# Optimization experiments

Measured on AMD Instinct MI355X. Metric: run time of the kernel, lower is better.

Reference implementation:

```python
import jax, jax.numpy as jnp
import numpy as np

B, W_DIM, CIN, COUT, K, H = 16, 512, 512, 512, 3, 64
PAD = (K - 1) // 2          # conv padding, also filtered_lrelu padding
GAIN = float(np.sqrt(2.0))  # lrelu gain (not torgb)
SLOPE = 0.2                 # lrelu slope (not torgb)
CLAMP = 256.0               # conv_clamp
AFFINE_WG = float(1.0 / np.sqrt(W_DIM))  # FullyConnectedLayer weight_gain


def setup_inputs() -> dict:
    key = jax.random.key(0)
    k0, k1, k2, k3 = jax.random.split(key, 4)
    return {
        "x": jax.random.normal(k0, (B, CIN, H, H), jnp.float32),
        "w": jax.random.normal(k1, (B, W_DIM), jnp.float32),
        "affine_weight": jax.random.normal(k2, (CIN, W_DIM), jnp.float32),
        "affine_bias": jnp.ones((CIN,), jnp.float32),       # bias_init=1
        "conv_weight": jax.random.normal(k3, (COUT, CIN, K, K), jnp.float32),
        "bias": jnp.zeros((COUT,), jnp.float32),
        "magnitude_ema": jnp.ones((), jnp.float32),
    }


def reference(x, w, affine_weight, affine_bias, conv_weight, bias, magnitude_ema):
    input_gain = jax.lax.rsqrt(magnitude_ema)
    # --- affine (FullyConnectedLayer, linear act, lr_mult=1) ---
    s = w @ (affine_weight * AFFINE_WG).T + affine_bias          # [B, CIN]
    # --- modulated_conv2d with demodulation (is_torgb=False) ---
    wk = conv_weight * jax.lax.rsqrt(
        jnp.mean(jnp.square(conv_weight), axis=(1, 2, 3), keepdims=True))
    s = s * jax.lax.rsqrt(jnp.mean(jnp.square(s)))
    wb = wk[None] * s[:, None, :, None, None]                    # [B,COUT,CIN,K,K]
    dcoefs = jax.lax.rsqrt(jnp.sum(jnp.square(wb), axis=(2, 3, 4)) + 1e-8)  # [B,COUT]
    wb = wb * dcoefs[:, :, None, None, None] * input_gain
    # grouped conv: groups = batch, one weight set per sample
    xg = x.reshape(1, B * CIN, H, H)
    wg = wb.reshape(B * COUT, CIN, K, K)
    y = jax.lax.conv_general_dilated(
        xg, wg, window_strides=(1, 1), padding=[(PAD, PAD), (PAD, PAD)],
        dimension_numbers=("NCHW", "OIHW", "NCHW"), feature_group_count=B)
    y = y.reshape(B, COUT, H, H)
    # --- filtered_lrelu: up=down=1, fu=fd=None (identity FIR) ---
    # => bias add, zero-pad by `padding`, lrelu * gain, clamp
    y = y + bias[:, None, None]
    y = jnp.pad(y, ((0, 0), (0, 0), (PAD, PAD), (PAD, PAD)))
    y = jnp.where(y >= 0, y, y * SLOPE) * GAIN
    y = jnp.clip(y, -CLAMP, CLAMP)                               # [B,COUT,66,66]
    return y
```

## Files before the change

### kernel.cpp

```cpp
#include <hip/hip_runtime.h>

#define B_     16
#define WDIM   512
#define CIN_   512
#define COUT_  512
#define HH     64
#define KC     32
#define NCHUNK (CIN_/KC)
#define AFFINE_WG 0.044194173824159216f
#define GAIN_  1.4142135623730951f
#define CLAMP_ 256.0f

#define WBYTES 36864
#define XBYTES 42240
#define BUFBYTES (WBYTES + XBYTES)

typedef __attribute__((ext_vector_type(4))) float f32x4;
typedef __attribute__((ext_vector_type(8))) short bf16x8;
typedef __attribute__((ext_vector_type(8))) unsigned short u16x8;

__device__ __forceinline__ unsigned short f2bf(float f) {
    union { float f; unsigned u; } un; un.f = f;
    unsigned u = un.u;
    u += 0x7FFFu + ((u >> 16) & 1u);
    return (unsigned short)(u >> 16);
}

__device__ __forceinline__ void gl_lds16(const void* g, void* l) {
    __builtin_amdgcn_global_load_lds(
        reinterpret_cast<const __attribute__((address_space(1))) unsigned int*>(
            reinterpret_cast<uintptr_t>(g)),
        reinterpret_cast<__attribute__((address_space(3))) unsigned int*>(
            reinterpret_cast<uintptr_t>(l)),
        16, 0, 0);
}


__global__ void k_affine(const float* __restrict__ w, const float* __restrict__ aw,
                         const float* __restrict__ ab, float* __restrict__ s,
                         float* __restrict__ part) {
    const int tid = threadIdx.x;
    const int b = blockIdx.x >> 1;
    const int c = ((blockIdx.x & 1) << 8) + tid;
    const f32x4* wr = (const f32x4*)(w + (size_t)b * WDIM);
    const f32x4* ar = (const f32x4*)(aw + (size_t)c * WDIM);
    float acc = 0.f;
    #pragma unroll 4
    for (int k = 0; k < WDIM / 4; ++k) {
        f32x4 a = ar[k], bb = wr[k];
        acc += a[0]*bb[0] + a[1]*bb[1] + a[2]*bb[2] + a[3]*bb[3];
    }
    float sv = acc * AFFINE_WG + ab[c];
    s[b * CIN_ + c] = sv;
    __shared__ float red[256];
    red[tid] = sv * sv;
    __syncthreads();
    for (int off = 128; off > 0; off >>= 1) {
        if (tid < off) red[tid] += red[tid + off];
        __syncthreads();
    }
    if (tid == 0) part[blockIdx.x] = red[0];
}

__global__ void k_wnorm(const float* __restrict__ cw, float* __restrict__ alpha,
                        float* __restrict__ Q) {
    const int o = blockIdx.x;
    const int tid = threadIdx.x;
    __shared__ float qsh[512];
    __shared__ float red[256];
    __shared__ float a_sh;
    float tot = 0.f;
    #pragma unroll
    for (int half = 0; half < 2; ++half) {
        const int c = tid + half * 256;
        const float* p = cw + ((size_t)o * 512 + c) * 9;
        float qs = 0.f;
        #pragma unroll
        for (int t = 0; t < 9; ++t) { float v = p[t]; qs += v * v; }
        qsh[c] = qs; tot += qs;
    }
    red[tid] = tot; __syncthreads();
    for (int off = 128; off > 0; off >>= 1) {
        if (tid < off) red[tid] += red[tid + off];
        __syncthreads();
    }
    if (tid == 0) { a_sh = rsqrtf(red[0] * (1.0f / 4608.0f)); alpha[o] = a_sh; }
    __syncthreads();
    const float a2 = a_sh * a_sh;
    Q[(size_t)o * 512 + tid]       = a2 * qsh[tid];
    Q[(size_t)o * 512 + tid + 256] = a2 * qsh[tid + 256];
}

__global__ void k_g(const float* __restrict__ s, const float* __restrict__ part,
                    const float* __restrict__ Q, const float* __restrict__ alpha,
                    const float* __restrict__ ema, float* __restrict__ g) {
    const int tid = threadIdx.x;
    const int b = blockIdx.x >> 1;
    const int o = ((blockIdx.x & 1) << 8) + tid;
    __shared__ float rs2_sh;
    if (tid == 0) {
        float t = 0.f;
        #pragma unroll
        for (int i = 0; i < 32; ++i) t += part[i];
        rs2_sh = 8192.0f / t;
    }
    __syncthreads();
    const f32x4* sh = (const f32x4*)(s + (size_t)b * CIN_);
    const f32x4* qq = (const f32x4*)(Q + (size_t)o * CIN_);
    float d = 0.f;
    #pragma unroll 4
    for (int k = 0; k < CIN_ / 4; ++k) {
        f32x4 a = sh[k], q4 = qq[k];
        d += a[0]*a[0]*q4[0] + a[1]*a[1]*q4[1] + a[2]*a[2]*q4[2] + a[3]*a[3]*q4[3];
    }
    const float ig = rsqrtf(ema[0]);
    g[b * COUT_ + o] = alpha[o] * rsqrtf(d * rs2_sh + 1e-8f) * ig;
}

__global__ void k_wprep2(const float* __restrict__ cw, unsigned short* __restrict__ wb) {
    const int S = blockIdx.x * 256 + threadIdx.x;
    const int p    = S / 2304;
    const int srem = S - p * 2304;
    const int a    = srem * 16;
    const int tap  = a >> 12;
    const int o    = (a >> 6) & 63;
    const int c0   = ((a & 63) ^ ((o & 6) << 3)) >> 1;
    const int ot = p >> 4, cc = p & 15;
    const int og = ot * 64 + o;
    const int cg = cc * 32 + c0;
    const float* src = cw + ((size_t)og * 512 + cg) * 9 + tap;
    u16x8 v;
    #pragma unroll
    for (int j = 0; j < 8; ++j) v[j] = f2bf(src[j * 9]);
    *(u16x8*)(wb + (size_t)S * 8) = v;
}

__global__ void k_xprep(const float* __restrict__ x, const float* __restrict__ s,
                        const float* __restrict__ part, unsigned short* __restrict__ xbf) {
    __shared__ float rs_sh;
    if (threadIdx.x == 0) {
        float t = 0.f;
        #pragma unroll
        for (int i = 0; i < 32; ++i) t += part[i];
        rs_sh = rsqrtf(t * (1.0f / 8192.0f));
    }
    __syncthreads();
    const float rs = rs_sh;
    const int slot = blockIdx.x * 256 + threadIdx.x;
    const int pair = slot >> 14;
    const int rem  = slot & 16383;
    const int row  = rem >> 8;
    const int ro16 = rem & 255;
    const int full = ro16 * 16 + 64;
    const int col  = full >> 6;
    const int c0   = ((full & 63) ^ ((col & 6) << 3)) >> 1;
    const int b    = pair >> 4, cc = pair & 15;
    const int cbase = cc * 32 + c0;
    const float* src = x + (((size_t)(b * CIN_ + cbase)) * HH + row) * HH + (col - 1);
    const float* sp  = s + b * CIN_ + cbase;
    u16x8 v;
    #pragma unroll
    for (int j = 0; j < 8; ++j)
        v[j] = f2bf(src[(size_t)j * 4096] * (sp[j] * rs));
    *(u16x8*)(xbf + (size_t)slot * 8) = v;
}

__global__ void k_border2(float* __restrict__ out) {
    const int f = blockIdx.x * 256 + threadIdx.x;
    const int bo = f / 132;
    const int r = f - bo * 132;
    const int row = (r >= 66) ? 65 : 0;
    const int col = (r >= 66) ? (r - 66) : r;
    out[(size_t)bo * 4356 + row * 66 + col] = 0.f;
}

__global__ __launch_bounds__(512, 2) void k_conv3(
    const unsigned short* __restrict__ xbf, const unsigned short* __restrict__ wb,
    const float* __restrict__ g, const float* __restrict__ bias,
    float* __restrict__ out) {
    __shared__ char lds[2 * BUFBYTES];

    const int tid  = threadIdx.x;
    const int lane = tid & 63;
    const int wv   = tid >> 6;
    const int l15  = lane & 15;
    const int hi   = lane >> 4;
    const int b  = blockIdx.z;
    const int ot = blockIdx.y;
    const int rt = blockIdx.x;
    const int h0 = rt * 8;

    const f32x4 zero4 = {0.f, 0.f, 0.f, 0.f};
    f32x4 acc[4][4];
    #pragma unroll
    for (int i = 0; i < 4; ++i)
        #pragma unroll
        for (int j = 0; j < 4; ++j) acc[i][j] = zero4;

    {
        unsigned int* x0 = (unsigned int*)(lds + WBYTES);
        unsigned int* x1 = (unsigned int*)(lds + BUFBYTES + WBYTES);
        for (int i = tid; i < XBYTES / 4; i += 512) { x0[i] = 0u; x1[i] = 0u; }
    }
    __syncthreads();

    const char* wsrc0 = (const char*)wb + (size_t)ot * 16 * WBYTES;
    const char* xsrc0 = (const char*)xbf + (size_t)b * 16 * 262144;

    auto STAGE = [&](int cc, char* base) {
        if (tid < 256) {
            const char* wsrc = wsrc0 + (size_t)cc * WBYTES;
            #pragma unroll
            for (int r = 0; r < 9; ++r)
                gl_lds16(wsrc + r * 4096 + tid * 16, base + r * 4096 + tid * 16);
        } else {
            const int t2 = tid - 256;
            const char* xsrc = xsrc0 + (size_t)cc * 262144;
            char* xb = base + WBYTES;
            #pragma unroll
            for (int r = 0; r < 10; ++r) {
                const int h_in = h0 - 1 + r;
                if ((unsigned)h_in < 64u)
                    gl_lds16(xsrc + (size_t)h_in * 4096 + t2 * 16,
                             xb + r * 4224 + 64 + t2 * 16);
            }
        }
    };

    STAGE(0, lds);
    __syncthreads();
    int cur = 0;

    for (int cc = 0; cc < NCHUNK; ++cc) {
        char* cbase = lds + cur * BUFBYTES;
        if (cc + 1 < NCHUNK) STAGE(cc + 1, lds + (cur ^ 1) * BUFBYTES);

        const char* Wl = cbase;
        const char* Xl = cbase + WBYTES;
        #pragma unroll
        for (int tap = 0; tap < 9; ++tap) {
            const int ti = tap / 3, tj = tap - ti * 3;
            bf16x8 af[4];
            #pragma unroll
            for (int mi = 0; mi < 4; ++mi) {
                const int o = mi * 16 + l15;
                int byte = (tap << 12) + (o << 6) + (hi << 4);
                byte ^= ((o & 6) << 3);
                af[mi] = *(const bf16x8*)(Wl + byte);
            }
            bf16x8 bg[4];
            const int row = wv + ti;
            #pragma unroll
            for (int ni = 0; ni < 4; ++ni) {
                const int col = ni * 16 + l15 + tj;
                int byte = (((row * 66 + col) << 5) + (hi << 3)) << 1;
                byte ^= ((col & 6) << 3);
                bg[ni] = *(const bf16x8*)(Xl + byte);
            }
            #pragma unroll
            for (int mi = 0; mi < 4; ++mi)
                #pragma unroll
                for (int ni = 0; ni < 4; ++ni)
                    acc[mi][ni] = __builtin_amdgcn_mfma_f32_16x16x32_bf16(
                        af[mi], bg[ni], acc[mi][ni], 0, 0, 0);
        }
        __syncthreads();
        cur ^= 1;
    }

    {
        const int obase = ot * 64;
        const int orow = h0 + wv + 1;
        #pragma unroll
        for (int mi = 0; mi < 4; ++mi) {
            #pragma unroll
            for (int r = 0; r < 4; ++r) {
                const int o = obase + mi * 16 + hi * 4 + r;
                const float gg = g[b * COUT_ + o];
                const float bb = bias[o];
                float* op = out + ((size_t)(b * COUT_ + o) * 66 + orow) * 66;
                #pragma unroll
                for (int ni = 0; ni < 4; ++ni) {
                    float v = acc[mi][ni][r] * gg + bb;
                    v = (v >= 0.f ? v : v * 0.2f) * GAIN_;
                    v = fminf(fmaxf(v, -CLAMP_), CLAMP_);
                    op[ni * 16 + l15 + 1] = v;
                }
                if (l15 == 0)  op[0]  = 0.f;
                if (l15 == 15) op[65] = 0.f;
            }
        }
    }
}

extern "C" void kernel_launch(void* const* d_in, const int* in_sizes, int n_in,
                              void* d_out, int out_size, void* d_ws, size_t ws_size,
                              hipStream_t stream) {
    const float* x    = (const float*)d_in[0];
    const float* w    = (const float*)d_in[1];
    const float* aw   = (const float*)d_in[2];
    const float* ab   = (const float*)d_in[3];
    const float* cw   = (const float*)d_in[4];
    const float* bias = (const float*)d_in[5];
    const float* ema  = (const float*)d_in[6];
    float* out = (float*)d_out;

    float* wsf   = (float*)d_ws;
    float* s     = wsf;
    float* part  = wsf + 8192;
    float* alpha = wsf + 16512;
    float* Q     = wsf + 17024;
    float* g     = wsf + 279168;
    unsigned short* wb  = (unsigned short*)((char*)d_ws + 1179648);
    unsigned short* xbf = (unsigned short*)((char*)d_ws + 5898240);

    k_affine <<<32, 256, 0, stream>>>(w, aw, ab, s, part);
    k_wnorm  <<<512, 256, 0, stream>>>(cw, alpha, Q);
    k_g      <<<32, 256, 0, stream>>>(s, part, Q, alpha, ema, g);
    k_wprep2 <<<1152, 256, 0, stream>>>(cw, wb);
    k_xprep  <<<16384, 256, 0, stream>>>(x, s, part, xbf);
    k_border2<<<4224, 256, 0, stream>>>(out);
    k_conv3  <<<dim3(8, 8, 16), 512, 0, stream>>>(xbf, wb, g, bias, out);
}
```

Before: 354.0 us.

## Coalesce x-prep via LDS tile, fuse border zeroing, remap conv blocks

The x preprocessing kernel now reads contiguous float4 rows per channel, transposes and swizzles them through a shared-memory tile, and writes bf16 output coalesced, replacing scattered strided reads. The border-zeroing kernel is folded into the conv kernel's epilogue for the top and bottom row tiles. The conv kernel uses a 1D grid remapped so neighbouring blocks are spread across batches and output tiles, likely for cache or XCD locality. It also unrolls double buffering into explicit A/B stages and adds an s_barrier mid-compute plus setprio around the MFMAs. Launch bounds drop to one block per SM, which may reduce occupancy.

```diff
diff --git a/kernel.cpp b/kernel.cpp
--- a/kernel.cpp
+++ b/kernel.cpp
@@ -13,7 +13,6 @@
 
 #define WBYTES 36864
 #define XBYTES 42240
-#define BUFBYTES (WBYTES + XBYTES)
 
 typedef __attribute__((ext_vector_type(4))) float f32x4;
 typedef __attribute__((ext_vector_type(8))) short bf16x8;
@@ -135,10 +134,12 @@
     *(u16x8*)(wb + (size_t)S * 8) = v;
 }
 
-__global__ void k_xprep(const float* __restrict__ x, const float* __restrict__ s,
-                        const float* __restrict__ part, unsigned short* __restrict__ xbf) {
+__global__ void k_xprep2(const float* __restrict__ x, const float* __restrict__ s,
+                         const float* __restrict__ part, unsigned short* __restrict__ xbf) {
     __shared__ float rs_sh;
-    if (threadIdx.x == 0) {
+    __shared__ char tile[8 * 4096];
+    const int tid = threadIdx.x;
+    if (tid == 0) {
         float t = 0.f;
         #pragma unroll
         for (int i = 0; i < 32; ++i) t += part[i];
@@ -146,48 +147,52 @@
     }
     __syncthreads();
     const float rs = rs_sh;
-    const int slot = blockIdx.x * 256 + threadIdx.x;
-    const int pair = slot >> 14;
-    const int rem  = slot & 16383;
-    const int row  = rem >> 8;
-    const int ro16 = rem & 255;
-    const int full = ro16 * 16 + 64;
-    const int col  = full >> 6;
-    const int c0   = ((full & 63) ^ ((col & 6) << 3)) >> 1;
-    const int b    = pair >> 4, cc = pair & 15;
-    const int cbase = cc * 32 + c0;
-    const float* src = x + (((size_t)(b * CIN_ + cbase)) * HH + row) * HH + (col - 1);
-    const float* sp  = s + b * CIN_ + cbase;
-    u16x8 v;
-    #pragma unroll
-    for (int j = 0; j < 8; ++j)
-        v[j] = f2bf(src[(size_t)j * 4096] * (sp[j] * rs));
-    *(u16x8*)(xbf + (size_t)slot * 8) = v;
-}
-
-__global__ void k_border2(float* __restrict__ out) {
-    const int f = blockIdx.x * 256 + threadIdx.x;
-    const int bo = f / 132;
-    const int r = f - bo * 132;
-    const int row = (r >= 66) ? 65 : 0;
-    const int col = (r >= 66) ? (r - 66) : r;
-    out[(size_t)bo * 4356 + row * 66 + col] = 0.f;
-}
-
-__global__ __launch_bounds__(512, 2) void k_conv3(
+    const int blk = blockIdx.x;
+    const int b  = blk >> 7;
+    const int cc = (blk >> 3) & 15;
+    const int rg = blk & 7;
+    const int c   = tid >> 3;
+    const int k8  = tid & 7;
+    const float sc = s[b * CIN_ + cc * 32 + c] * rs;
+    const float* src = x + (((size_t)(b * CIN_ + cc * 32 + c)) * HH + rg * 8) * HH + k8 * 8;
+    #pragma unroll
+    for (int row = 0; row < 8; ++row) {
+        const f32x4 v0 = *(const f32x4*)(src + (size_t)row * HH);
+        const f32x4 v1 = *(const f32x4*)(src + (size_t)row * HH + 4);
+        #pragma unroll
+        for (int q = 0; q < 8; ++q) {
+            const float v = (q < 4) ? v0[q] : v1[q - 4];
+            const int col = k8 * 8 + q + 1;
+            const int byte = ((col * 64 + 2 * c) ^ ((col & 6) << 3)) - 64;
+            *(unsigned short*)(tile + row * 4096 + byte) = f2bf(v * sc);
+        }
+    }
+    __syncthreads();
+    unsigned short* dst = xbf + ((size_t)(b * 16 + cc) * 64 + rg * 8) * 2048;
+    const u16x8* tsrc = (const u16x8*)tile;
+    #pragma unroll
+    for (int k = 0; k < 8; ++k)
+        *(u16x8*)(dst + (size_t)(tid + k * 256) * 8) = tsrc[tid + k * 256];
+}
+
+__global__ __launch_bounds__(512, 1) void k_conv4(
     const unsigned short* __restrict__ xbf, const unsigned short* __restrict__ wb,
     const float* __restrict__ g, const float* __restrict__ bias,
     float* __restrict__ out) {
-    __shared__ char lds[2 * BUFBYTES];
+    __shared__ char bufA[WBYTES + XBYTES];
+    __shared__ char bufB[WBYTES + XBYTES];
 
     const int tid  = threadIdx.x;
     const int lane = tid & 63;
     const int wv   = tid >> 6;
     const int l15  = lane & 15;
     const int hi   = lane >> 4;
-    const int b  = blockIdx.z;
-    const int ot = blockIdx.y;
-    const int rt = blockIdx.x;
+
+    const int orig = blockIdx.x;
+    const int wg = (orig & 7) * 128 + (orig >> 3);
+    const int b  = wg >> 6;
+    const int ot = (wg >> 3) & 7;
+    const int rt = wg & 7;
     const int h0 = rt * 8;
 
     const f32x4 zero4 = {0.f, 0.f, 0.f, 0.f};
@@ -198,8 +203,8 @@
         for (int j = 0; j < 4; ++j) acc[i][j] = zero4;
 
     {
-        unsigned int* x0 = (unsigned int*)(lds + WBYTES);
-        unsigned int* x1 = (unsigned int*)(lds + BUFBYTES + WBYTES);
+        unsigned int* x0 = (unsigned int*)(bufA + WBYTES);
+        unsigned int* x1 = (unsigned int*)(bufB + WBYTES);
         for (int i = tid; i < XBYTES / 4; i += 512) { x0[i] = 0u; x1[i] = 0u; }
     }
     __syncthreads();
@@ -207,7 +212,7 @@
     const char* wsrc0 = (const char*)wb + (size_t)ot * 16 * WBYTES;
     const char* xsrc0 = (const char*)xbf + (size_t)b * 16 * 262144;
 
-    auto STAGE = [&](int cc, char* base) {
+    auto STAGE = [&](char* base, int cc) {
         if (tid < 256) {
             const char* wsrc = wsrc0 + (size_t)cc * WBYTES;
             #pragma unroll
@@ -227,16 +232,7 @@
         }
     };
 
-    STAGE(0, lds);
-    __syncthreads();
-    int cur = 0;
-
-    for (int cc = 0; cc < NCHUNK; ++cc) {
-        char* cbase = lds + cur * BUFBYTES;
-        if (cc + 1 < NCHUNK) STAGE(cc + 1, lds + (cur ^ 1) * BUFBYTES);
-
-        const char* Wl = cbase;
-        const char* Xl = cbase + WBYTES;
+    auto COMPUTE = [&](const char* Wl, const char* Xl) {
         #pragma unroll
         for (int tap = 0; tap < 9; ++tap) {
             const int ti = tap / 3, tj = tap - ti * 3;
@@ -257,15 +253,30 @@
                 byte ^= ((col & 6) << 3);
                 bg[ni] = *(const bf16x8*)(Xl + byte);
             }
+            if (tap == 5) __builtin_amdgcn_s_barrier();
+            __builtin_amdgcn_s_setprio(1);
             #pragma unroll
             for (int mi = 0; mi < 4; ++mi)
                 #pragma unroll
                 for (int ni = 0; ni < 4; ++ni)
                     acc[mi][ni] = __builtin_amdgcn_mfma_f32_16x16x32_bf16(
                         af[mi], bg[ni], acc[mi][ni], 0, 0, 0);
-        }
+            __builtin_amdgcn_s_setprio(0);
+        }
+    };
+
+    STAGE(bufA, 0);
+    __syncthreads();
+
+    #pragma unroll 1
+    for (int it = 0; it < 8; ++it) {
+        const int cc = it * 2;
+        STAGE(bufB, cc + 1);
+        COMPUTE(bufA, bufA + WBYTES);
         __syncthreads();
-        cur ^= 1;
+        if (cc + 2 < NCHUNK) STAGE(bufA, cc + 2);
+        COMPUTE(bufB, bufB + WBYTES);
+        __syncthreads();
     }
 
     {
@@ -290,6 +301,13 @@
                 if (l15 == 15) op[65] = 0.f;
             }
         }
+        if (rt == 0 || rt == 7) {
+            const int row = (rt == 0) ? 0 : 65;
+            for (int i = tid; i < 64 * 66; i += 512) {
+                const int o = obase + i / 66, col = i - (i / 66) * 66;
+                out[((size_t)(b * COUT_ + o) * 66 + row) * 66 + col] = 0.f;
+            }
+        }
     }
 }
 
@@ -318,7 +336,6 @@
     k_wnorm  <<<512, 256, 0, stream>>>(cw, alpha, Q);
     k_g      <<<32, 256, 0, stream>>>(s, part, Q, alpha, ema, g);
     k_wprep2 <<<1152, 256, 0, stream>>>(cw, wb);
-    k_xprep  <<<16384, 256, 0, stream>>>(x, s, part, xbf);
-    k_border2<<<4224, 256, 0, stream>>>(out);
-    k_conv3  <<<dim3(8, 8, 16), 512, 0, stream>>>(xbf, wb, g, bias, out);
-}
+    k_xprep2 <<<2048, 256, 0, stream>>>(x, s, part, xbf);
+    k_conv4  <<<1024, 512, 0, stream>>>(xbf, wb, g, bias, out);
+}
```

New measurement: 342.1 us. 1.03x faster.
